# Optimization experiments

Hardware: AMD Instinct MI355X
Metric: run time of the kernel (lower is better)

## Reference

```python
import jax, jax.numpy as jnp
import numpy as np

GMAX, EMAX, NATOM, AA = 4, 10, 14, 20
SCALE_CLAMP = 0.1
EPS = 1e-8


def setup_inputs() -> dict:
    key = jax.random.key(0)
    ks = jax.random.split(key, 10)
    B, N, H = 4, 16384, 256
    rng = np.random.default_rng(0)
    # per-AA kinematic metadata (mimics pack_residue_meta_for_batch output)
    G_counts = rng.integers(1, GMAX + 1, size=AA).astype(np.int32)
    tors_axis = np.full((AA, GMAX, 2), -1, np.int32)
    aff_idx = np.zeros((AA, GMAX, EMAX), np.int32)
    aff_mask = np.zeros((AA, GMAX, EMAX), bool)
    for a in range(AA):
        for g in range(int(G_counts[a])):
            tors_axis[a, g] = rng.permutation(NATOM)[:2]
            perm = rng.permutation(NATOM)[:EMAX]  # unique affected atoms
            ne = int(rng.integers(3, EMAX + 1))
            aff_idx[a, g, :ne] = perm[:ne]
            aff_mask[a, g, :ne] = True
    scale_mask = rng.random((AA, NATOM)) < 0.5
    scale_parent = rng.integers(0, NATOM, size=(AA, NATOM)).astype(np.int32)

    s = 0.05
    ap = jax.random.uniform(ks[1], (B, N, AA), jnp.float32)
    return {
        'h': jax.random.normal(ks[0], (B, N, H), jnp.float32),
        'aatype_probs': ap / ap.sum(-1, keepdims=True),
        'X': jax.random.normal(ks[2], (B, N, NATOM, 3), jnp.float32),
        'W1': jax.random.normal(ks[3], (H + AA, H), jnp.float32) * s,
        'b1': jnp.zeros((H,), jnp.float32),
        'W2': jax.random.normal(ks[4], (H, H), jnp.float32) * s,
        'b2': jnp.zeros((H,), jnp.float32),
        'Wt': jax.random.normal(ks[5], (H, GMAX), jnp.float32) * s,
        'bt': jnp.zeros((GMAX,), jnp.float32),
        'Ws': jax.random.normal(ks[6], (H, NATOM), jnp.float32) * s,
        'bs': jnp.zeros((NATOM,), jnp.float32),
        'exists': jax.random.uniform(ks[7], (B, N, NATOM)) < 0.9,
        'top_idx': jax.random.randint(ks[8], (B, N), 0, AA, jnp.int32),
        'tors_axis': jnp.asarray(tors_axis),
        'aff_idx': jnp.asarray(aff_idx),
        'aff_mask': jnp.asarray(aff_mask),
        'G_counts': jnp.asarray(G_counts),
        'scale_mask': jnp.asarray(scale_mask),
        'scale_parent': jnp.asarray(scale_parent),
    }


def _take(X, idx):
    # X: [B,N,14,3], idx: [B,N,K] -> [B,N,K,3]
    return jnp.take_along_axis(X, jnp.broadcast_to(idx[..., None], idx.shape + (3,)), axis=2)


def _fk(X, exists, dchi, sraw, top_idx, TA, AI, AM, GC, SM, SP):
    B, N = top_idx.shape
    bi = jnp.arange(B)[:, None, None]
    ni = jnp.arange(N)[None, :, None]
    g_mask = jnp.arange(GMAX) < GC[..., None]  # [B,N,Gmax]
    for gi in range(GMAX):
        u, v = TA[..., gi, 0], TA[..., gi, 1]
        axis_ok = (u >= 0) & (v >= 0) & g_mask[..., gi]
        Pu = _take(X, jnp.maximum(u, 0)[..., None])  # [B,N,1,3]
        Pv = _take(X, jnp.maximum(v, 0)[..., None])
        axis = Pv - Pu
        axisn = axis / jnp.maximum(jnp.linalg.norm(axis, axis=-1, keepdims=True), EPS)
        ang = jnp.where(axis_ok, dchi[..., gi], 0.0)[..., None, None]  # [B,N,1,1]
        cols = jnp.maximum(AI[..., gi, :], 0)  # [B,N,E]
        cmask = AM[..., gi, :]
        Xa = _take(X, cols)          # [B,N,E,3]
        Va = Xa - Pu
        cos, sin = jnp.cos(ang), jnp.sin(ang)
        cross = jnp.cross(jnp.broadcast_to(axisn, Va.shape), Va, axis=-1)
        dot = jnp.sum(Va * axisn, -1, keepdims=True)
        Xa_new = Pu + Va * cos + cross * sin + axisn * dot * (1.0 - cos)
        ex_cols = jnp.take_along_axis(exists, cols, axis=2)
        wmask = cmask & ex_cols
        safe_cols = jnp.where(wmask, cols, NATOM)  # OOB -> dropped
        X = X.at[bi, ni, safe_cols].set(Xa_new, mode='drop')
    # bond-length scaling toward parent atom
    SPc = jnp.maximum(SP, 0)
    Pp = _take(X, SPc)               # [B,N,14,3]
    vvec = X - Pp
    r = jnp.maximum(jnp.linalg.norm(vvec, axis=-1, keepdims=True), EPS)
    dirv = vvec / r
    s_eff = jnp.clip(sraw, -1.0, 1.0) * SCALE_CLAMP
    Pa_new = Pp + dirv * r * (1.0 + s_eff[..., None])
    pair_exist = exists & jnp.take_along_axis(exists, SPc, axis=2)
    W = (SM & pair_exist)[..., None]
    return jnp.where(W, Pa_new, X)


def reference(h, aatype_probs, X, W1, b1, W2, b2, Wt, bt, Ws, bs,
              exists, top_idx, tors_axis, aff_idx, aff_mask, G_counts,
              scale_mask, scale_parent):
    # TorsionScaleHead
    z = jnp.concatenate([h, aatype_probs], axis=-1)
    z = jax.nn.silu(z @ W1 + b1)
    z = jax.nn.silu(z @ W2 + b2)
    dchi = jnp.tanh(z @ Wt + bt) * 0.5      # [B,N,Gmax]
    sraw = jnp.tanh(z @ Ws + bs)            # [B,N,14]
    # gather per-residue metadata
    TA = tors_axis[top_idx]
    AI = aff_idx[top_idx]
    AM = aff_mask[top_idx]
    GC = G_counts[top_idx]
    SM = scale_mask[top_idx]
    SP = scale_parent[top_idx]
    return _fk(X, exists, dchi, sraw, top_idx, TA, AI, AM, GC, SM, SP)
```

## Files before the change

### kernel.cpp

```cpp
#include <hip/hip_runtime.h>
#include <hip/hip_bf16.h>
#include <stdint.h>

#define TM 64
#define NT 512
#define HDIM 256
#define HA 276
#define HAP 288
#define ZROW 296
#define AAC 20
#define GMAXC 4
#define EMAXC 10
#define NATOMC 14

#define W1T_OFF 0
#define W2T_OFF 73728
#define W3T_OFF 139264
#define WS_ELEMS 147456

#define ZH_OFF  0
#define ZL_OFF  37888
#define XS_OFF  37888
#define EXS_OFF 48640
#define TSS_OFF 75776
#define SMEM_BYTES 80640

typedef __attribute__((ext_vector_type(8))) short bf16x8;
typedef __attribute__((ext_vector_type(4))) short short4v;
typedef __attribute__((ext_vector_type(4))) float f32x4;

__device__ __forceinline__ float silu_f(float x) {
    return x * (1.0f / (1.0f + __expf(-x)));
}

__device__ __forceinline__ float tanh_fast(float x) {
    float e = __expf(2.0f * x);
    return 1.0f - 2.0f / (e + 1.0f);
}

__device__ __forceinline__ unsigned short f2bf(float f) {
    union { float f; unsigned int u; } x; x.f = f;
    unsigned int r = x.u + 0x7fffu + ((x.u >> 16) & 1u);
    return (unsigned short)(r >> 16);
}

__device__ __forceinline__ float bf2f(unsigned short s) {
    union { unsigned int u; float f; } x; x.u = ((unsigned int)s) << 16;
    return x.f;
}

template <bool SPLIT>
__global__ __launch_bounds__(256) void prep_weights(
    const float* __restrict__ W1, const float* __restrict__ W2,
    const float* __restrict__ Wt, const float* __restrict__ Ws,
    unsigned short* __restrict__ ws)
{
    int idx = blockIdx.x * 256 + threadIdx.x;
    if (idx >= WS_ELEMS) return;
    float v;
    if (idx < W2T_OFF) {
        int n = idx / HAP, k = idx - n * HAP;
        v = (k < HA) ? W1[(size_t)k * HDIM + n] : 0.0f;
    } else if (idx < W3T_OFF) {
        int i = idx - W2T_OFF;
        int n = i / HDIM, k = i - n * HDIM;
        v = W2[(size_t)k * HDIM + n];
    } else {
        int i = idx - W3T_OFF;
        int n = i / HDIM, k = i - n * HDIM;
        v = (n < GMAXC) ? Wt[(size_t)k * GMAXC + n]
          : (n < GMAXC + NATOMC) ? Ws[(size_t)k * NATOMC + (n - GMAXC)]
          : 0.0f;
    }
    unsigned short hi = f2bf(v);
    ws[idx] = hi;
    if (SPLIT) ws[WS_ELEMS + idx] = f2bf(v - bf2f(hi));
}

template <bool SPLIT>
__global__ __launch_bounds__(NT, 4) void fused_refiner(
    const float* __restrict__ h,
    const float* __restrict__ probs,
    const float* __restrict__ X,
    const unsigned short* __restrict__ ws,
    const float* __restrict__ b1,
    const float* __restrict__ b2,
    const float* __restrict__ bt,
    const float* __restrict__ bs,
    const int* __restrict__ exists,
    const int* __restrict__ top_idx,
    const int* __restrict__ TA,
    const int* __restrict__ AI,
    const int* __restrict__ AM,
    const int* __restrict__ GC,
    const int* __restrict__ SM,
    const int* __restrict__ SP,
    float* __restrict__ out)
{
    __shared__ __align__(16) unsigned char smem[SMEM_BYTES];
    unsigned short (*zh)[ZROW] = (unsigned short (*)[ZROW])(smem + ZH_OFF);
    unsigned short (*zl)[ZROW] = (unsigned short (*)[ZROW])(smem + ZL_OFF);
    float (*tsS)[19]           = (float (*)[19])(smem + TSS_OFF);
    float (*Xs)[NATOMC][3]     = (float (*)[NATOMC][3])(smem + XS_OFF);
    uint8_t (*exS)[NATOMC]     = (uint8_t (*)[NATOMC])(smem + EXS_OFF);

    const int tid  = threadIdx.x;
    const int tok0 = blockIdx.x * TM;

    const int wv   = tid >> 6;
    const int ln   = tid & 63;
    const int ln16 = ln & 15;
    const int kg   = ln >> 4;
    const int nc0  = wv * 32;

    {
        const float4* h4 = reinterpret_cast<const float4*>(h + (size_t)tok0 * HDIM);
        for (int idx = tid; idx < TM * (HDIM / 4); idx += NT) {
            int t  = idx >> 6;
            int kq = idx & 63;
            float4 v = h4[(size_t)t * (HDIM / 4) + kq];
            short4v sh, sl;
            unsigned short a;
            a = f2bf(v.x); sh.x = (short)a; sl.x = (short)f2bf(v.x - bf2f(a));
            a = f2bf(v.y); sh.y = (short)a; sl.y = (short)f2bf(v.y - bf2f(a));
            a = f2bf(v.z); sh.z = (short)a; sl.z = (short)f2bf(v.z - bf2f(a));
            a = f2bf(v.w); sh.w = (short)a; sl.w = (short)f2bf(v.w - bf2f(a));
            *reinterpret_cast<short4v*>(&zh[t][kq * 4]) = sh;
            *reinterpret_cast<short4v*>(&zl[t][kq * 4]) = sl;
        }
        for (int idx = tid; idx < TM * AAC; idx += NT) {
            int t = idx / AAC;
            int p = idx - t * AAC;
            float v = probs[(size_t)(tok0 + t) * AAC + p];
            unsigned short a = f2bf(v);
            zh[t][HDIM + p] = a;
            zl[t][HDIM + p] = f2bf(v - bf2f(a));
        }
        for (int idx = tid; idx < TM * (ZROW - HA); idx += NT) {
            int t = idx / (ZROW - HA);
            int p = idx - t * (ZROW - HA);
            zh[t][HA + p] = 0;
            zl[t][HA + p] = 0;
        }
    }
    __syncthreads();

    const unsigned short* Wh = ws;
    const unsigned short* Wl = ws + WS_ELEMS;

    {
        f32x4 acc[4][2];
        #pragma unroll
        for (int m = 0; m < 4; ++m)
            #pragma unroll
            for (int n = 0; n < 2; ++n) acc[m][n] = (f32x4){0.f, 0.f, 0.f, 0.f};

        const size_t wbase = (size_t)(nc0 + ln16) * HAP + kg * 8 + W1T_OFF;
        bf16x8 nbh0 = *reinterpret_cast<const bf16x8*>(Wh + wbase);
        bf16x8 nbh1 = *reinterpret_cast<const bf16x8*>(Wh + wbase + 16 * HAP);
        bf16x8 nbl0 = {}, nbl1 = {};
        if (SPLIT) {
            nbl0 = *reinterpret_cast<const bf16x8*>(Wl + wbase);
            nbl1 = *reinterpret_cast<const bf16x8*>(Wl + wbase + 16 * HAP);
        }
        #pragma unroll
        for (int kc = 0; kc < 9; ++kc) {
            const bf16x8 bh0 = nbh0, bh1 = nbh1, bl0 = nbl0, bl1 = nbl1;
            if (kc + 1 < 9) {
                const size_t wn = wbase + (size_t)(kc + 1) * 32;
                nbh0 = *reinterpret_cast<const bf16x8*>(Wh + wn);
                nbh1 = *reinterpret_cast<const bf16x8*>(Wh + wn + 16 * HAP);
                if (SPLIT) {
                    nbl0 = *reinterpret_cast<const bf16x8*>(Wl + wn);
                    nbl1 = *reinterpret_cast<const bf16x8*>(Wl + wn + 16 * HAP);
                }
            }
            const int kk = kc * 32 + kg * 8;
            bf16x8 ah[4], al[4];
            #pragma unroll
            for (int m = 0; m < 4; ++m) {
                ah[m] = *reinterpret_cast<const bf16x8*>(&zh[m * 16 + ln16][kk]);
                al[m] = *reinterpret_cast<const bf16x8*>(&zl[m * 16 + ln16][kk]);
            }
            #pragma unroll
            for (int m = 0; m < 4; ++m)
                acc[m][0] = __builtin_amdgcn_mfma_f32_16x16x32_bf16(ah[m], bh0, acc[m][0], 0, 0, 0);
            #pragma unroll
            for (int m = 0; m < 4; ++m)
                acc[m][0] = __builtin_amdgcn_mfma_f32_16x16x32_bf16(al[m], bh0, acc[m][0], 0, 0, 0);
            if (SPLIT) {
                #pragma unroll
                for (int m = 0; m < 4; ++m)
                    acc[m][0] = __builtin_amdgcn_mfma_f32_16x16x32_bf16(ah[m], bl0, acc[m][0], 0, 0, 0);
            }
            #pragma unroll
            for (int m = 0; m < 4; ++m)
                acc[m][1] = __builtin_amdgcn_mfma_f32_16x16x32_bf16(ah[m], bh1, acc[m][1], 0, 0, 0);
            #pragma unroll
            for (int m = 0; m < 4; ++m)
                acc[m][1] = __builtin_amdgcn_mfma_f32_16x16x32_bf16(al[m], bh1, acc[m][1], 0, 0, 0);
            if (SPLIT) {
                #pragma unroll
                for (int m = 0; m < 4; ++m)
                    acc[m][1] = __builtin_amdgcn_mfma_f32_16x16x32_bf16(ah[m], bl1, acc[m][1], 0, 0, 0);
            }
        }
        __syncthreads();
        #pragma unroll
        for (int n = 0; n < 2; ++n) {
            const int col = nc0 + n * 16 + ln16;
            const float bias = b1[col];
            #pragma unroll
            for (int m = 0; m < 4; ++m) {
                #pragma unroll
                for (int r = 0; r < 4; ++r) {
                    const int row = m * 16 + kg * 4 + r;
                    float val = silu_f(acc[m][n][r] + bias);
                    unsigned short hi = f2bf(val);
                    zh[row][col] = hi;
                    zl[row][col] = f2bf(val - bf2f(hi));
                }
            }
        }
    }
    __syncthreads();

    {
        f32x4 acc[4][2];
        #pragma unroll
        for (int m = 0; m < 4; ++m)
            #pragma unroll
            for (int n = 0; n < 2; ++n) acc[m][n] = (f32x4){0.f, 0.f, 0.f, 0.f};

        const size_t wbase = (size_t)(nc0 + ln16) * HDIM + kg * 8 + W2T_OFF;
        bf16x8 nbh0 = *reinterpret_cast<const bf16x8*>(Wh + wbase);
        bf16x8 nbh1 = *reinterpret_cast<const bf16x8*>(Wh + wbase + 16 * HDIM);
        bf16x8 nbl0 = {}, nbl1 = {};
        if (SPLIT) {
            nbl0 = *reinterpret_cast<const bf16x8*>(Wl + wbase);
            nbl1 = *reinterpret_cast<const bf16x8*>(Wl + wbase + 16 * HDIM);
        }
        #pragma unroll
        for (int kc = 0; kc < 8; ++kc) {
            const bf16x8 bh0 = nbh0, bh1 = nbh1, bl0 = nbl0, bl1 = nbl1;
            if (kc + 1 < 8) {
                const size_t wn = wbase + (size_t)(kc + 1) * 32;
                nbh0 = *reinterpret_cast<const bf16x8*>(Wh + wn);
                nbh1 = *reinterpret_cast<const bf16x8*>(Wh + wn + 16 * HDIM);
                if (SPLIT) {
                    nbl0 = *reinterpret_cast<const bf16x8*>(Wl + wn);
                    nbl1 = *reinterpret_cast<const bf16x8*>(Wl + wn + 16 * HDIM);
                }
            }
            const int kk = kc * 32 + kg * 8;
            bf16x8 ah[4], al[4];
            #pragma unroll
            for (int m = 0; m < 4; ++m) {
                ah[m] = *reinterpret_cast<const bf16x8*>(&zh[m * 16 + ln16][kk]);
                al[m] = *reinterpret_cast<const bf16x8*>(&zl[m * 16 + ln16][kk]);
            }
            #pragma unroll
            for (int m = 0; m < 4; ++m)
                acc[m][0] = __builtin_amdgcn_mfma_f32_16x16x32_bf16(ah[m], bh0, acc[m][0], 0, 0, 0);
            #pragma unroll
            for (int m = 0; m < 4; ++m)
                acc[m][0] = __builtin_amdgcn_mfma_f32_16x16x32_bf16(al[m], bh0, acc[m][0], 0, 0, 0);
            if (SPLIT) {
                #pragma unroll
                for (int m = 0; m < 4; ++m)
                    acc[m][0] = __builtin_amdgcn_mfma_f32_16x16x32_bf16(ah[m], bl0, acc[m][0], 0, 0, 0);
            }
            #pragma unroll
            for (int m = 0; m < 4; ++m)
                acc[m][1] = __builtin_amdgcn_mfma_f32_16x16x32_bf16(ah[m], bh1, acc[m][1], 0, 0, 0);
            #pragma unroll
            for (int m = 0; m < 4; ++m)
                acc[m][1] = __builtin_amdgcn_mfma_f32_16x16x32_bf16(al[m], bh1, acc[m][1], 0, 0, 0);
            if (SPLIT) {
                #pragma unroll
                for (int m = 0; m < 4; ++m)
                    acc[m][1] = __builtin_amdgcn_mfma_f32_16x16x32_bf16(ah[m], bl1, acc[m][1], 0, 0, 0);
            }
        }
        __syncthreads();
        #pragma unroll
        for (int n = 0; n < 2; ++n) {
            const int col = nc0 + n * 16 + ln16;
            const float bias = b2[col];
            #pragma unroll
            for (int m = 0; m < 4; ++m) {
                #pragma unroll
                for (int r = 0; r < 4; ++r) {
                    const int row = m * 16 + kg * 4 + r;
                    float val = silu_f(acc[m][n][r] + bias);
                    unsigned short hi = f2bf(val);
                    zh[row][col] = hi;
                    zl[row][col] = f2bf(val - bf2f(hi));
                }
            }
        }
    }
    __syncthreads();

    {
        const int m3 = wv & 3;
        const int n3 = wv >> 2;
        f32x4 acc = (f32x4){0.f, 0.f, 0.f, 0.f};
        const size_t wbase = (size_t)(n3 * 16 + ln16) * HDIM + kg * 8 + W3T_OFF;
        #pragma unroll
        for (int kc = 0; kc < 8; ++kc) {
            const int kk = kc * 32 + kg * 8;
            bf16x8 ah = *reinterpret_cast<const bf16x8*>(&zh[m3 * 16 + ln16][kk]);
            bf16x8 al = *reinterpret_cast<const bf16x8*>(&zl[m3 * 16 + ln16][kk]);
            const size_t wo = wbase + kc * 32;
            bf16x8 bh = *reinterpret_cast<const bf16x8*>(Wh + wo);
            acc = __builtin_amdgcn_mfma_f32_16x16x32_bf16(ah, bh, acc, 0, 0, 0);
            acc = __builtin_amdgcn_mfma_f32_16x16x32_bf16(al, bh, acc, 0, 0, 0);
            if (SPLIT) {
                bf16x8 bl = *reinterpret_cast<const bf16x8*>(Wl + wo);
                acc = __builtin_amdgcn_mfma_f32_16x16x32_bf16(ah, bl, acc, 0, 0, 0);
            }
        }
        const int o = n3 * 16 + ln16;
        if (o < GMAXC + NATOMC) {
            const float bias = (o < GMAXC) ? bt[o] : bs[o - GMAXC];
            #pragma unroll
            for (int r = 0; r < 4; ++r) {
                const int tok = m3 * 16 + kg * 4 + r;
                float val = tanh_fast(acc[r] + bias);
                if (o < GMAXC) val *= 0.5f;
                tsS[tok][o] = val;
            }
        }
    }
    __syncthreads();

    {
        float* Xsf = &Xs[0][0][0];
        for (int idx = tid; idx < TM * NATOMC * 3; idx += NT) {
            Xsf[idx] = X[(size_t)tok0 * NATOMC * 3 + idx];
        }
        uint8_t* exf = &exS[0][0];
        for (int idx = tid; idx < TM * NATOMC; idx += NT) {
            exf[idx] = (uint8_t)(exists[(size_t)tok0 * NATOMC + idx] != 0);
        }
    }
    __syncthreads();

    {
        const int t_loc = ln >> 3;
        const int r     = ln & 7;
        const int t     = wv * 8 + t_loc;
        const int a     = top_idx[tok0 + t];

        for (int gi = 0; gi < GMAXC; ++gi) {
            const int u  = TA[a * 8 + gi * 2 + 0];
            const int v  = TA[a * 8 + gi * 2 + 1];
            const int gc = GC[a];
            const bool axis_ok = (u >= 0) && (v >= 0) && (gi < gc);
            const int iu = u > 0 ? u : 0;
            const int iv = v > 0 ? v : 0;
            const float pux = Xs[t][iu][0], puy = Xs[t][iu][1], puz = Xs[t][iu][2];
            float ax = Xs[t][iv][0] - pux;
            float ay = Xs[t][iv][1] - puy;
            float az = Xs[t][iv][2] - puz;
            const float nrm = sqrtf(ax * ax + ay * ay + az * az);
            const float inv = 1.0f / fmaxf(nrm, 1e-8f);
            const float nx = ax * inv, ny = ay * inv, nz = az * inv;
            const float ang = axis_ok ? tsS[t][gi] : 0.0f;
            float sn, cs;
            __sincosf(ang, &sn, &cs);
            const float omc = 1.0f - cs;

            float newp[2][3];
            int   cidx[2];
            bool  wf[2];
            #pragma unroll
            for (int q = 0; q < 2; ++q) {
                const int e = r + q * 8;
                wf[q] = false; cidx[q] = 0;
                if (e < EMAXC) {
                    const int craw = AI[a * 40 + gi * 10 + e];
                    const int c = craw > 0 ? craw : 0;
                    const bool m = AM[a * 40 + gi * 10 + e] != 0;
                    const float vx = Xs[t][c][0] - pux;
                    const float vy = Xs[t][c][1] - puy;
                    const float vz = Xs[t][c][2] - puz;
                    const float dt  = vx * nx + vy * ny + vz * nz;
                    const float crx = ny * vz - nz * vy;
                    const float cry = nz * vx - nx * vz;
                    const float crz = nx * vy - ny * vx;
                    newp[q][0] = pux + vx * cs + crx * sn + nx * dt * omc;
                    newp[q][1] = puy + vy * cs + cry * sn + ny * dt * omc;
                    newp[q][2] = puz + vz * cs + crz * sn + nz * dt * omc;
                    const bool exc = exS[t][c] != 0;
                    wf[q] = m && exc;
                    cidx[q] = c;
                }
            }
            #pragma unroll
            for (int q = 0; q < 2; ++q) {
                if (wf[q]) {
                    Xs[t][cidx[q]][0] = newp[q][0];
                    Xs[t][cidx[q]][1] = newp[q][1];
                    Xs[t][cidx[q]][2] = newp[q][2];
                }
            }
        }

        #pragma unroll
        for (int q = 0; q < 2; ++q) {
            const int e = r + q * 8;
            if (e < NATOMC) {
                const int praw = SP[a * 14 + e];
                const int p = praw > 0 ? praw : 0;
                const float ppx = Xs[t][p][0], ppy = Xs[t][p][1], ppz = Xs[t][p][2];
                const float vx = Xs[t][e][0] - ppx;
                const float vy = Xs[t][e][1] - ppy;
                const float vz = Xs[t][e][2] - ppz;
                const float sr = tsS[t][GMAXC + e];
                const float se = fminf(fmaxf(sr, -1.f), 1.f) * 0.1f;
                const float f = 1.0f + se;
                const bool w = (SM[a * 14 + e] != 0) && (exS[t][e] != 0) && (exS[t][p] != 0);
                const float ox = w ? (ppx + vx * f) : Xs[t][e][0];
                const float oy = w ? (ppy + vy * f) : Xs[t][e][1];
                const float oz = w ? (ppz + vz * f) : Xs[t][e][2];
                const size_t ob = ((size_t)(tok0 + t) * NATOMC + e) * 3;
                out[ob + 0] = ox;
                out[ob + 1] = oy;
                out[ob + 2] = oz;
            }
        }
    }
}

extern "C" void kernel_launch(void* const* d_in, const int* in_sizes, int n_in,
                              void* d_out, int out_size, void* d_ws, size_t ws_size,
                              hipStream_t stream) {
    const float* h      = (const float*)d_in[0];
    const float* probs  = (const float*)d_in[1];
    const float* X      = (const float*)d_in[2];
    const float* W1     = (const float*)d_in[3];
    const float* b1     = (const float*)d_in[4];
    const float* W2     = (const float*)d_in[5];
    const float* b2     = (const float*)d_in[6];
    const float* Wt     = (const float*)d_in[7];
    const float* bt     = (const float*)d_in[8];
    const float* Ws     = (const float*)d_in[9];
    const float* bs     = (const float*)d_in[10];
    const int*   exists = (const int*)d_in[11];
    const int*   tidx   = (const int*)d_in[12];
    const int*   TA     = (const int*)d_in[13];
    const int*   AI     = (const int*)d_in[14];
    const int*   AM     = (const int*)d_in[15];
    const int*   GC     = (const int*)d_in[16];
    const int*   SM     = (const int*)d_in[17];
    const int*   SP     = (const int*)d_in[18];
    float*       out    = (float*)d_out;
    unsigned short* ws  = (unsigned short*)d_ws;

    const int BN = in_sizes[12];
    const int grid = BN / TM;
    const size_t need_split = (size_t)2 * WS_ELEMS * sizeof(unsigned short);

    if (ws_size >= need_split) {
        prep_weights<true><<<(WS_ELEMS + 255) / 256, 256, 0, stream>>>(W1, W2, Wt, Ws, ws);
        fused_refiner<true><<<grid, NT, 0, stream>>>(h, probs, X, ws, b1, b2, bt, bs,
                                                     exists, tidx, TA, AI, AM, GC, SM, SP, out);
    } else {
        prep_weights<false><<<(WS_ELEMS + 255) / 256, 256, 0, stream>>>(W1, W2, Wt, Ws, ws);
        fused_refiner<false><<<grid, NT, 0, stream>>>(h, probs, X, ws, b1, b2, bt, bs,
                                                      exists, tidx, TA, AI, AM, GC, SM, SP, out);
    }
}
```

Before: 105.3 us.

## Double token tile to 128 with 1024 threads and truncate low-bf16 split

Raises the per-block token tile from 64 to 128 and the block size from 512 to 1024 threads. Waves are split into two row halves so that each weight fragment loaded from global memory serves twice as many tokens, halving weight traffic per token. Shared memory grows to about 158 KB, which limits occupancy to one block per CU, and launch_bounds(256) may now conflict with the 1024-thread launch. The low part of the bf16 split now uses truncation instead of rounding to save a few ALU ops, at a slight cost in accuracy.

```diff
diff --git a/kernel.cpp b/kernel.cpp
--- a/kernel.cpp
+++ b/kernel.cpp
@@ -2,8 +2,8 @@
 #include <hip/hip_bf16.h>
 #include <stdint.h>
 
-#define TM 64
-#define NT 512
+#define TM 128
+#define NT 1024
 #define HDIM 256
 #define HA 276
 #define HAP 288
@@ -19,11 +19,11 @@
 #define WS_ELEMS 147456
 
 #define ZH_OFF  0
-#define ZL_OFF  37888
-#define XS_OFF  37888
-#define EXS_OFF 48640
-#define TSS_OFF 75776
-#define SMEM_BYTES 80640
+#define ZL_OFF  75776
+#define XS_OFF  75776
+#define EXS_OFF 97280
+#define TSS_OFF 151552
+#define SMEM_BYTES 161280
 
 typedef __attribute__((ext_vector_type(8))) short bf16x8;
 typedef __attribute__((ext_vector_type(4))) short short4v;
@@ -42,6 +42,11 @@
     union { float f; unsigned int u; } x; x.f = f;
     unsigned int r = x.u + 0x7fffu + ((x.u >> 16) & 1u);
     return (unsigned short)(r >> 16);
+}
+
+__device__ __forceinline__ unsigned short f2bf_trunc(float f) {
+    union { float f; unsigned int u; } x; x.f = f;
+    return (unsigned short)(x.u >> 16);
 }
 
 __device__ __forceinline__ float bf2f(unsigned short s) {
@@ -111,7 +116,9 @@
     const int ln   = tid & 63;
     const int ln16 = ln & 15;
     const int kg   = ln >> 4;
-    const int nc0  = wv * 32;
+    const int mh   = wv & 1;
+    const int nc0  = (wv >> 1) * 32;
+    const int row0 = mh * 64;
 
     {
         const float4* h4 = reinterpret_cast<const float4*>(h + (size_t)tok0 * HDIM);
@@ -121,10 +128,10 @@
             float4 v = h4[(size_t)t * (HDIM / 4) + kq];
             short4v sh, sl;
             unsigned short a;
-            a = f2bf(v.x); sh.x = (short)a; sl.x = (short)f2bf(v.x - bf2f(a));
-            a = f2bf(v.y); sh.y = (short)a; sl.y = (short)f2bf(v.y - bf2f(a));
-            a = f2bf(v.z); sh.z = (short)a; sl.z = (short)f2bf(v.z - bf2f(a));
-            a = f2bf(v.w); sh.w = (short)a; sl.w = (short)f2bf(v.w - bf2f(a));
+            a = f2bf(v.x); sh.x = (short)a; sl.x = (short)f2bf_trunc(v.x - bf2f(a));
+            a = f2bf(v.y); sh.y = (short)a; sl.y = (short)f2bf_trunc(v.y - bf2f(a));
+            a = f2bf(v.z); sh.z = (short)a; sl.z = (short)f2bf_trunc(v.z - bf2f(a));
+            a = f2bf(v.w); sh.w = (short)a; sl.w = (short)f2bf_trunc(v.w - bf2f(a));
             *reinterpret_cast<short4v*>(&zh[t][kq * 4]) = sh;
             *reinterpret_cast<short4v*>(&zl[t][kq * 4]) = sl;
         }
@@ -134,7 +141,7 @@
             float v = probs[(size_t)(tok0 + t) * AAC + p];
             unsigned short a = f2bf(v);
             zh[t][HDIM + p] = a;
-            zl[t][HDIM + p] = f2bf(v - bf2f(a));
+            zl[t][HDIM + p] = f2bf_trunc(v - bf2f(a));
         }
         for (int idx = tid; idx < TM * (ZROW - HA); idx += NT) {
             int t = idx / (ZROW - HA);
@@ -179,8 +186,8 @@
             bf16x8 ah[4], al[4];
             #pragma unroll
             for (int m = 0; m < 4; ++m) {
-                ah[m] = *reinterpret_cast<const bf16x8*>(&zh[m * 16 + ln16][kk]);
-                al[m] = *reinterpret_cast<const bf16x8*>(&zl[m * 16 + ln16][kk]);
+                ah[m] = *reinterpret_cast<const bf16x8*>(&zh[row0 + m * 16 + ln16][kk]);
+                al[m] = *reinterpret_cast<const bf16x8*>(&zl[row0 + m * 16 + ln16][kk]);
             }
             #pragma unroll
             for (int m = 0; m < 4; ++m)
@@ -214,11 +221,11 @@
             for (int m = 0; m < 4; ++m) {
                 #pragma unroll
                 for (int r = 0; r < 4; ++r) {
-                    const int row = m * 16 + kg * 4 + r;
+                    const int row = row0 + m * 16 + kg * 4 + r;
                     float val = silu_f(acc[m][n][r] + bias);
                     unsigned short hi = f2bf(val);
                     zh[row][col] = hi;
-                    zl[row][col] = f2bf(val - bf2f(hi));
+                    zl[row][col] = f2bf_trunc(val - bf2f(hi));
                 }
             }
         }
@@ -256,8 +263,8 @@
             bf16x8 ah[4], al[4];
             #pragma unroll
             for (int m = 0; m < 4; ++m) {
-                ah[m] = *reinterpret_cast<const bf16x8*>(&zh[m * 16 + ln16][kk]);
-                al[m] = *reinterpret_cast<const bf16x8*>(&zl[m * 16 + ln16][kk]);
+                ah[m] = *reinterpret_cast<const bf16x8*>(&zh[row0 + m * 16 + ln16][kk]);
+                al[m] = *reinterpret_cast<const bf16x8*>(&zl[row0 + m * 16 + ln16][kk]);
             }
             #pragma unroll
             for (int m = 0; m < 4; ++m)
@@ -291,11 +298,11 @@
             for (int m = 0; m < 4; ++m) {
                 #pragma unroll
                 for (int r = 0; r < 4; ++r) {
-                    const int row = m * 16 + kg * 4 + r;
+                    const int row = row0 + m * 16 + kg * 4 + r;
                     float val = silu_f(acc[m][n][r] + bias);
                     unsigned short hi = f2bf(val);
                     zh[row][col] = hi;
-                    zl[row][col] = f2bf(val - bf2f(hi));
+                    zl[row][col] = f2bf_trunc(val - bf2f(hi));
                 }
             }
         }
@@ -303,8 +310,8 @@
     __syncthreads();
 
     {
-        const int m3 = wv & 3;
-        const int n3 = wv >> 2;
+        const int m3 = wv & 7;
+        const int n3 = wv >> 3;
         f32x4 acc = (f32x4){0.f, 0.f, 0.f, 0.f};
         const size_t wbase = (size_t)(n3 * 16 + ln16) * HDIM + kg * 8 + W3T_OFF;
         #pragma unroll
@@ -348,10 +355,9 @@
     __syncthreads();
 
     {
-        const int t_loc = ln >> 3;
-        const int r     = ln & 7;
-        const int t     = wv * 8 + t_loc;
-        const int a     = top_idx[tok0 + t];
+        const int t = tid >> 3;
+        const int r = tid & 7;
+        const int a = top_idx[tok0 + t];
 
         for (int gi = 0; gi < GMAXC; ++gi) {
             const int u  = TA[a * 8 + gi * 2 + 0];
```

Result: slower. 117.2 us (+11.3%).
